# Performance work log

Measured on AMD Instinct MI355X. Metric: run time of the kernel, lower is better.

Reference implementation:

```python
import jax, jax.numpy as jnp
import numpy as np

C_Z = 128
C_HIDDEN = 128
EPS = 1e-5


def _layer_norm(x, w, b):
    mu = jnp.mean(x, axis=-1, keepdims=True)
    var = jnp.var(x, axis=-1, keepdims=True)
    return (x - mu) * jax.lax.rsqrt(var + EPS) * w + b


def setup_inputs() -> dict:
    key = jax.random.key(0)
    ks = jax.random.split(key, 8)
    B, N = 1, 384
    z = jax.random.normal(ks[0], (B, N, N, C_Z), dtype=jnp.float32)
    mask = jnp.ones((B, N, N), dtype=jnp.float32)
    s_z = 1.0 / np.sqrt(C_Z)
    s_h = 1.0 / np.sqrt(C_HIDDEN)
    return {
        "z": z,
        "mask": mask,
        # projection linears (lecun-like random init)
        "w_ap": jax.random.normal(ks[1], (C_HIDDEN, C_Z), jnp.float32) * s_z,
        "b_ap": jnp.zeros((C_HIDDEN,), jnp.float32),
        "w_bp": jax.random.normal(ks[2], (C_HIDDEN, C_Z), jnp.float32) * s_z,
        "b_bp": jnp.zeros((C_HIDDEN,), jnp.float32),
        # gating linears: torch init is zeros weight / ones bias, but use small
        # random weights so gradients are non-trivial; bias = 1 as in 'gating' init
        "w_ag": jax.random.normal(ks[3], (C_HIDDEN, C_Z), jnp.float32) * s_z,
        "b_ag": jnp.ones((C_HIDDEN,), jnp.float32),
        "w_bg": jax.random.normal(ks[4], (C_HIDDEN, C_Z), jnp.float32) * s_z,
        "b_bg": jnp.ones((C_HIDDEN,), jnp.float32),
        "w_g": jax.random.normal(ks[5], (C_Z, C_Z), jnp.float32) * s_z,
        "b_g": jnp.ones((C_Z,), jnp.float32),
        # final output linear ('final' init is zeros; randomize for a useful baseline)
        "w_z": jax.random.normal(ks[6], (C_Z, C_HIDDEN), jnp.float32) * s_h,
        "b_z": jnp.zeros((C_Z,), jnp.float32),
        "ln_in_w": jnp.ones((C_Z,), jnp.float32),
        "ln_in_b": jnp.zeros((C_Z,), jnp.float32),
        "ln_out_w": jnp.ones((C_HIDDEN,), jnp.float32),
        "ln_out_b": jnp.zeros((C_HIDDEN,), jnp.float32),
    }


def reference(z, mask, w_ap, b_ap, w_bp, b_bp, w_ag, b_ag, w_bg, b_bg,
              w_g, b_g, w_z, b_z, ln_in_w, ln_in_b, ln_out_w, ln_out_b):
    # z: [B, N, N, C_z], mask: [B, N, N]
    m = mask[..., None]
    zn = _layer_norm(z, ln_in_w, ln_in_b)
    a = (zn @ w_ap.T + b_ap) * jax.nn.sigmoid(zn @ w_ag.T + b_ag) * m
    b = (zn @ w_bp.T + b_bp) * jax.nn.sigmoid(zn @ w_bg.T + b_bg) * m
    # outgoing: a -> [B,C,i,j], b -> [B,C,j,i]
    a_p = jnp.transpose(a, (0, 3, 1, 2))
    b_p = jnp.transpose(b, (0, 3, 2, 1))
    # NOTE: repo's einsum has no contracted index -> elementwise product a*b
    x = jnp.einsum('bcij,bcji->bijc', a_p, b_p)  # [B, N, N, C_hidden]
    x = _layer_norm(x, ln_out_w, ln_out_b)
    x = x @ w_z.T + b_z
    g = jax.nn.sigmoid(zn @ w_g.T + b_g)
    return x * g
```

## Files before the change

### kernel.cpp

```cpp
#include <hip/hip_runtime.h>
#include <hip/hip_bf16.h>

#define NN 384
#define CC 128
#define PP (NN*NN)
#define PB 64
#define NB (PP/PB)
#define TPB 256

typedef __attribute__((ext_vector_type(8))) short bf16x8;
typedef __attribute__((ext_vector_type(4))) float f32x4;
typedef __attribute__((ext_vector_type(8))) unsigned short u16x8;


__device__ __forceinline__ unsigned short f2bf(float f){
  __hip_bfloat16 h = __float2bfloat16(f);
  return __builtin_bit_cast(unsigned short, h);
}
__device__ __forceinline__ float bf2f(unsigned h){ return __uint_as_float(h<<16); }
__device__ __forceinline__ unsigned pack2(float a, float b){
  return (unsigned)f2bf(a) | ((unsigned)f2bf(b)<<16);
}
__device__ __forceinline__ float sigmoidf_(float x){
  return __fdividef(1.0f, 1.0f + __expf(-x));
}

__global__ __launch_bounds__(256) void k0_wprep(
    const float* __restrict__ wap, const float* __restrict__ wag,
    const float* __restrict__ wbp, const float* __restrict__ wbg,
    const float* __restrict__ wg,  const float* __restrict__ wz,
    unsigned short* __restrict__ wfrag){
  int tid = blockIdx.x*256 + threadIdx.x;
  int plane = tid >> 11, chunk = tid & 2047;
  const float* W = (plane==0) ? wag
                 : (plane==1||plane==2) ? wap
                 : (plane==3) ? wbg
                 : (plane==4||plane==5) ? wbp
                 : (plane==6) ? wg : wz;
  bool lo = (plane==2)||(plane==5);
  int k0 = chunk >> 9, n = (chunk >> 6) & 7, l = chunk & 63;
  int o  = n*16 + (l & 15);
  int kb = k0*32 + ((l>>4)<<3);
  const float* s = W + o*128 + kb;
  u16x8 v;
  #pragma unroll
  for (int e=0;e<8;e++){
    float w = s[e];
    unsigned short hh = f2bf(w);
    v[e] = lo ? f2bf(w - bf2f(hh)) : hh;
  }
  *(u16x8*)(wfrag + (size_t)tid*8) = v;
}

__device__ __forceinline__ void stage_q(const unsigned char* __restrict__ src_base,
                                        unsigned char* slot, int t){
  int wv = t>>6, l = t&63;
  const unsigned char* src = src_base + wv*2048 + l*16;
  unsigned char* dst = slot + wv*2048;
  #pragma unroll
  for (int i=0;i<2;i++)
    __builtin_amdgcn_global_load_lds(
        (const __attribute__((address_space(1))) unsigned int*)(src + i*1024),
        (__attribute__((address_space(3))) unsigned int*)(dst + i*1024),
        16, 0, 0);
}

__device__ __forceinline__ void q_H(const bf16x8* a, int q,
    const unsigned char* slot, int l, f32x4* acc){
  #pragma unroll
  for (int n=0;n<8;n++){
    bf16x8 f = *(const bf16x8*)(slot + n*1024 + l*16);
    acc[n] = __builtin_amdgcn_mfma_f32_16x16x32_bf16(a[q], f, acc[n], 0,0,0);
  }
}
__device__ __forceinline__ void q_HL(const bf16x8* aH, const bf16x8* aL, int q,
    const unsigned char* slot, int l, f32x4* acc){
  #pragma unroll
  for (int n=0;n<8;n++){
    bf16x8 f = *(const bf16x8*)(slot + n*1024 + l*16);
    acc[n] = __builtin_amdgcn_mfma_f32_16x16x32_bf16(aH[q], f, acc[n], 0,0,0);
    acc[n] = __builtin_amdgcn_mfma_f32_16x16x32_bf16(aL[q], f, acc[n], 0,0,0);
  }
}
__device__ __forceinline__ void bias_init(const float* __restrict__ b, int cb,
                                          f32x4* acc){
  #pragma unroll
  for (int n=0;n<8;n++){
    float v = b[n*16 + cb];
    f32x4 iv = {v,v,v,v};
    acc[n]=iv;
  }
}
__device__ __forceinline__ void extract4(const unsigned char* base, int row0,
                                         int l, bf16x8 a[4]){
  int row = row0 + (l&15);
  int swz = (row&7)<<4;
  #pragma unroll
  for (int k0=0;k0<4;k0++){
    unsigned off = (unsigned)(row*256 + ((((l>>4)<<4) + (k0<<6)) ^ swz));
    a[k0] = *(const bf16x8*)(base + off);
  }
}

__global__ __launch_bounds__(TPB,2) void k_fused(
    const float* __restrict__ z, const float* __restrict__ mask,
    const float* __restrict__ bap, const float* __restrict__ bag,
    const float* __restrict__ bbp, const float* __restrict__ bbg,
    const float* __restrict__ bgg, const float* __restrict__ bz,
    const float* __restrict__ lniw, const float* __restrict__ lnib,
    const float* __restrict__ lnow, const float* __restrict__ lnob,
    const unsigned short* __restrict__ wfrag,
    float* __restrict__ out){
  __shared__ unsigned char lds[32768];
  unsigned char* buf = lds;
  const unsigned char* wfrag8 = (const unsigned char*)wfrag;
  const int t = threadIdx.x;
  const int pos0 = blockIdx.x * PB;
  const int wv = t>>6, l = t&63;
  const int h2 = (t>>5)&1;
  const int c4 = (t&31)<<2;
  const int row0 = wv*16;

  stage_q(wfrag8, lds + 16384, t);

  unsigned plr[16];
  {
    float4 lw = *(const float4*)(lniw + c4);
    float4 lb = *(const float4*)(lnib + c4);
    #pragma unroll
    for (int it=0; it<8; ++it){
      int row = row0 + it*2 + h2;
      float4 v = *(const float4*)(z + (size_t)(pos0+row)*CC + c4);
      float s = v.x+v.y+v.z+v.w;
      #pragma unroll
      for (int mm=1; mm<32; mm<<=1) s += __shfl_xor(s,mm);
      float mu = s*(1.0f/128.0f);
      float d0=v.x-mu, d1=v.y-mu, d2=v.z-mu, d3=v.w-mu;
      float ss = d0*d0+d1*d1+d2*d2+d3*d3;
      #pragma unroll
      for (int mm=1; mm<32; mm<<=1) ss += __shfl_xor(ss,mm);
      float rstd = rsqrtf(ss*(1.0f/128.0f) + 1e-5f);
      float n0=d0*rstd*lw.x+lb.x, n1=d1*rstd*lw.y+lb.y;
      float n2=d2*rstd*lw.z+lb.z, n3=d3*rstd*lw.w+lb.w;
      unsigned short hh0=f2bf(n0), hh1=f2bf(n1), hh2=f2bf(n2), hh3=f2bf(n3);
      unsigned off = (unsigned)(row*256 + ((c4<<1) ^ ((row&7)<<4)));
      *(uint2*)(buf + off) = make_uint2((unsigned)hh0|((unsigned)hh1<<16),
                                        (unsigned)hh2|((unsigned)hh3<<16));
      plr[it*2]   = pack2(n0-bf2f(hh0), n1-bf2f(hh1));
      plr[it*2+1] = pack2(n2-bf2f(hh2), n3-bf2f(hh3));
    }
  }
  bf16x8 aH[4], aLo[4];
  extract4(buf, row0, l, aH);
  #pragma unroll
  for (int it=0; it<8; ++it){
    int row = row0 + it*2 + h2;
    unsigned off = (unsigned)(row*256 + ((c4<<1) ^ ((row&7)<<4)));
    *(uint2*)(buf + off) = make_uint2(plr[it*2], plr[it*2+1]);
  }
  extract4(buf, row0, l, aLo);

  const int cb = l&15;
  const int g4 = (l>>4)<<2;

  float mk[4];
  #pragma unroll
  for (int r=0;r<4;r++) mk[r] = mask[pos0 + row0 + g4 + r];

  f32x4 gA[8], gB[8], prj[8];

#define SL(p) (lds + 16384 + (((p)&1)<<13))
#define PH(p) do{ __syncthreads(); \
    if ((p)+1 < 32) stage_q(wfrag8 + ((size_t)((p)+1))*8192, SL((p)+1), t); }while(0)
#define SIG_INPLACE(A) do{ \
    _Pragma("unroll") \
    for (int n=0;n<8;n++) \
      _Pragma("unroll") \
      for (int r=0;r<4;r++) (A)[n][r] = sigmoidf_((A)[n][r]); \
  }while(0)

  PH(0);  bias_init(bag,cb,gA); q_H(aH,0,SL(0), l,gA);
  PH(1);  q_H(aH,1,SL(1), l,gA);
  PH(2);  q_H(aH,2,SL(2), l,gA);
  PH(3);  q_H(aH,3,SL(3), l,gA);
  SIG_INPLACE(gA);
  PH(4);  bias_init(bap,cb,prj); q_HL(aH,aLo,0,SL(4), l,prj);
  PH(5);  q_HL(aH,aLo,1,SL(5), l,prj);
  PH(6);  q_HL(aH,aLo,2,SL(6), l,prj);
  PH(7);  q_HL(aH,aLo,3,SL(7), l,prj);
  PH(8);  q_H(aH,0,SL(8), l,prj);
  PH(9);  q_H(aH,1,SL(9), l,prj);
  PH(10); q_H(aH,2,SL(10),l,prj);
  PH(11); q_H(aH,3,SL(11),l,prj);
  #pragma unroll
  for (int n=0;n<8;n++)
    #pragma unroll
    for (int r=0;r<4;r++)
      gA[n][r] = prj[n][r]*gA[n][r]*mk[r];
  PH(12); bias_init(bbg,cb,gB); q_H(aH,0,SL(12),l,gB);
  PH(13); q_H(aH,1,SL(13),l,gB);
  PH(14); q_H(aH,2,SL(14),l,gB);
  PH(15); q_H(aH,3,SL(15),l,gB);
  SIG_INPLACE(gB);
  PH(16); bias_init(bbp,cb,prj); q_HL(aH,aLo,0,SL(16),l,prj);
  PH(17); q_HL(aH,aLo,1,SL(17),l,prj);
  PH(18); q_HL(aH,aLo,2,SL(18),l,prj);
  PH(19); q_HL(aH,aLo,3,SL(19),l,prj);
  PH(20); q_H(aH,0,SL(20),l,prj);
  PH(21); q_H(aH,1,SL(21),l,prj);
  PH(22); q_H(aH,2,SL(22),l,prj);
  PH(23); q_H(aH,3,SL(23),l,prj);
  bf16x8 a2[4];
  {
    #pragma unroll
    for (int n=0;n<8;n++)
      #pragma unroll
      for (int r=0;r<4;r++)
        gA[n][r] *= prj[n][r]*gB[n][r]*mk[r];
    float lw8[8], lb8[8];
    #pragma unroll
    for (int n=0;n<8;n++){ lw8[n]=lnow[n*16+cb]; lb8[n]=lnob[n*16+cb]; }
    #pragma unroll
    for (int r=0;r<4;r++){
      float s=0.f;
      #pragma unroll
      for (int n=0;n<8;n++) s += gA[n][r];
      #pragma unroll
      for (int mm=1; mm<16; mm<<=1) s += __shfl_xor(s,mm);
      float mu = s*(1.0f/128.0f);
      float ss=0.f;
      #pragma unroll
      for (int n=0;n<8;n++){ float d = gA[n][r]-mu; ss += d*d; }
      #pragma unroll
      for (int mm=1; mm<16; mm<<=1) ss += __shfl_xor(ss,mm);
      float rstd = rsqrtf(ss*(1.0f/128.0f) + 1e-5f);
      int row = row0 + g4 + r;
      int swz = (row&7)<<4;
      #pragma unroll
      for (int n=0;n<8;n++){
        int colb = (n*16+cb)*2;
        float vvv = (gA[n][r]-mu)*rstd*lw8[n]+lb8[n];
        *(unsigned short*)(buf + row*256 + (colb ^ swz)) = f2bf(vvv);
      }
    }
    extract4(buf, row0, l, a2);
  }
  PH(24); bias_init(bgg,cb,gB); q_H(aH,0,SL(24),l,gB);
  PH(25); q_H(aH,1,SL(25),l,gB);
  PH(26); q_H(aH,2,SL(26),l,gB);
  PH(27); q_H(aH,3,SL(27),l,gB);
  SIG_INPLACE(gB);
  PH(28); bias_init(bz,cb,prj); q_H(a2,0,SL(28),l,prj);
  PH(29); q_H(a2,1,SL(29),l,prj);
  PH(30); q_H(a2,2,SL(30),l,prj);
  PH(31); q_H(a2,3,SL(31),l,prj);
  #pragma unroll
  for (int n=0;n<8;n++){
    #pragma unroll
    for (int r=0;r<4;r++){
      int row = row0 + g4 + r;
      out[(size_t)(pos0+row)*CC + n*16 + cb] = prj[n][r]*gB[n][r];
    }
  }
#undef PH
#undef SL
#undef SIG_INPLACE
}

extern "C" void kernel_launch(void* const* d_in, const int* in_sizes, int n_in,
                              void* d_out, int out_size, void* d_ws, size_t ws_size,
                              hipStream_t stream){
  const float* z     = (const float*)d_in[0];
  const float* mask  = (const float*)d_in[1];
  const float* w_ap  = (const float*)d_in[2];
  const float* b_ap  = (const float*)d_in[3];
  const float* w_bp  = (const float*)d_in[4];
  const float* b_bp  = (const float*)d_in[5];
  const float* w_ag  = (const float*)d_in[6];
  const float* b_ag  = (const float*)d_in[7];
  const float* w_bg  = (const float*)d_in[8];
  const float* b_bg  = (const float*)d_in[9];
  const float* w_g   = (const float*)d_in[10];
  const float* b_g   = (const float*)d_in[11];
  const float* w_z   = (const float*)d_in[12];
  const float* b_z   = (const float*)d_in[13];
  const float* ln_in_w  = (const float*)d_in[14];
  const float* ln_in_b  = (const float*)d_in[15];
  const float* ln_out_w = (const float*)d_in[16];
  const float* ln_out_b = (const float*)d_in[17];

  unsigned short* wfrag = (unsigned short*)d_ws;

  k0_wprep<<<64, 256, 0, stream>>>(w_ap, w_ag, w_bp, w_bg, w_g, w_z, wfrag);
  k_fused<<<NB, TPB, 0, stream>>>(z, mask, b_ap, b_ag, b_bp, b_bg, b_g, b_z,
                                  ln_in_w, ln_in_b, ln_out_w, ln_out_b,
                                  wfrag, (float*)d_out);
}
```

Measured before the change: 111.2 us.

## Read weight fragments straight from global memory instead of LDS double-buffering

Drops the 32-phase LDS staging pipeline, which used global_load_lds with a __syncthreads per phase. Each wave now loads its bf16 weight fragments directly from global memory, relying on L1/L2 caching of the 256KB fragment array, inside fully unrolled per-projection passes. This removes 32 block-wide barriers and halves LDS use to 16KB. In exchange, every wave issues its own global loads for the same weights, and load latency is no longer hidden by explicit prefetch.

```diff
diff --git a/kernel.cpp b/kernel.cpp
--- a/kernel.cpp
+++ b/kernel.cpp
@@ -52,34 +52,27 @@
   *(u16x8*)(wfrag + (size_t)tid*8) = v;
 }
 
-__device__ __forceinline__ void stage_q(const unsigned char* __restrict__ src_base,
-                                        unsigned char* slot, int t){
-  int wv = t>>6, l = t&63;
-  const unsigned char* src = src_base + wv*2048 + l*16;
-  unsigned char* dst = slot + wv*2048;
-  #pragma unroll
-  for (int i=0;i<2;i++)
-    __builtin_amdgcn_global_load_lds(
-        (const __attribute__((address_space(1))) unsigned int*)(src + i*1024),
-        (__attribute__((address_space(3))) unsigned int*)(dst + i*1024),
-        16, 0, 0);
-}
-
-__device__ __forceinline__ void q_H(const bf16x8* a, int q,
-    const unsigned char* slot, int l, f32x4* acc){
-  #pragma unroll
-  for (int n=0;n<8;n++){
-    bf16x8 f = *(const bf16x8*)(slot + n*1024 + l*16);
-    acc[n] = __builtin_amdgcn_mfma_f32_16x16x32_bf16(a[q], f, acc[n], 0,0,0);
-  }
-}
-__device__ __forceinline__ void q_HL(const bf16x8* aH, const bf16x8* aL, int q,
-    const unsigned char* slot, int l, f32x4* acc){
-  #pragma unroll
-  for (int n=0;n<8;n++){
-    bf16x8 f = *(const bf16x8*)(slot + n*1024 + l*16);
-    acc[n] = __builtin_amdgcn_mfma_f32_16x16x32_bf16(aH[q], f, acc[n], 0,0,0);
-    acc[n] = __builtin_amdgcn_mfma_f32_16x16x32_bf16(aL[q], f, acc[n], 0,0,0);
+__device__ __forceinline__ void pass_Hg(const bf16x8* a,
+    const unsigned char* __restrict__ wp, int l, f32x4* acc){
+  #pragma unroll
+  for (int q=0;q<4;q++){
+    #pragma unroll
+    for (int n=0;n<8;n++){
+      bf16x8 f = *(const bf16x8*)(wp + q*8192 + n*1024 + l*16);
+      acc[n] = __builtin_amdgcn_mfma_f32_16x16x32_bf16(a[q], f, acc[n], 0,0,0);
+    }
+  }
+}
+__device__ __forceinline__ void pass_HLg(const bf16x8* aH, const bf16x8* aL,
+    const unsigned char* __restrict__ wp, int l, f32x4* acc){
+  #pragma unroll
+  for (int q=0;q<4;q++){
+    #pragma unroll
+    for (int n=0;n<8;n++){
+      bf16x8 f = *(const bf16x8*)(wp + q*8192 + n*1024 + l*16);
+      acc[n] = __builtin_amdgcn_mfma_f32_16x16x32_bf16(aH[q], f, acc[n], 0,0,0);
+      acc[n] = __builtin_amdgcn_mfma_f32_16x16x32_bf16(aL[q], f, acc[n], 0,0,0);
+    }
   }
 }
 __device__ __forceinline__ void bias_init(const float* __restrict__ b, int cb,
@@ -111,17 +104,14 @@
     const float* __restrict__ lnow, const float* __restrict__ lnob,
     const unsigned short* __restrict__ wfrag,
     float* __restrict__ out){
-  __shared__ unsigned char lds[32768];
-  unsigned char* buf = lds;
-  const unsigned char* wfrag8 = (const unsigned char*)wfrag;
+  __shared__ unsigned char buf[16384];
+  const unsigned char* wf = (const unsigned char*)wfrag;
   const int t = threadIdx.x;
   const int pos0 = blockIdx.x * PB;
   const int wv = t>>6, l = t&63;
-  const int h2 = (t>>5)&1;
+  const int hg = (t>>5)&1;
   const int c4 = (t&31)<<2;
   const int row0 = wv*16;
-
-  stage_q(wfrag8, lds + 16384, t);
 
   unsigned plr[16];
   {
@@ -129,7 +119,7 @@
     float4 lb = *(const float4*)(lnib + c4);
     #pragma unroll
     for (int it=0; it<8; ++it){
-      int row = row0 + it*2 + h2;
+      int row = row0 + it*2 + hg;
       float4 v = *(const float4*)(z + (size_t)(pos0+row)*CC + c4);
       float s = v.x+v.y+v.z+v.w;
       #pragma unroll
@@ -154,7 +144,7 @@
   extract4(buf, row0, l, aH);
   #pragma unroll
   for (int it=0; it<8; ++it){
-    int row = row0 + it*2 + h2;
+    int row = row0 + it*2 + hg;
     unsigned off = (unsigned)(row*256 + ((c4<<1) ^ ((row&7)<<4)));
     *(uint2*)(buf + off) = make_uint2(plr[it*2], plr[it*2+1]);
   }
@@ -169,9 +159,6 @@
 
   f32x4 gA[8], gB[8], prj[8];
 
-#define SL(p) (lds + 16384 + (((p)&1)<<13))
-#define PH(p) do{ __syncthreads(); \
-    if ((p)+1 < 32) stage_q(wfrag8 + ((size_t)((p)+1))*8192, SL((p)+1), t); }while(0)
 #define SIG_INPLACE(A) do{ \
     _Pragma("unroll") \
     for (int n=0;n<8;n++) \
@@ -179,37 +166,21 @@
       for (int r=0;r<4;r++) (A)[n][r] = sigmoidf_((A)[n][r]); \
   }while(0)
 
-  PH(0);  bias_init(bag,cb,gA); q_H(aH,0,SL(0), l,gA);
-  PH(1);  q_H(aH,1,SL(1), l,gA);
-  PH(2);  q_H(aH,2,SL(2), l,gA);
-  PH(3);  q_H(aH,3,SL(3), l,gA);
+  bias_init(bag,cb,gA); pass_Hg(aH, wf + 0*32768, l, gA);
   SIG_INPLACE(gA);
-  PH(4);  bias_init(bap,cb,prj); q_HL(aH,aLo,0,SL(4), l,prj);
-  PH(5);  q_HL(aH,aLo,1,SL(5), l,prj);
-  PH(6);  q_HL(aH,aLo,2,SL(6), l,prj);
-  PH(7);  q_HL(aH,aLo,3,SL(7), l,prj);
-  PH(8);  q_H(aH,0,SL(8), l,prj);
-  PH(9);  q_H(aH,1,SL(9), l,prj);
-  PH(10); q_H(aH,2,SL(10),l,prj);
-  PH(11); q_H(aH,3,SL(11),l,prj);
+  bias_init(bap,cb,prj);
+  pass_HLg(aH, aLo, wf + 1*32768, l, prj);
+  pass_Hg (aH,      wf + 2*32768, l, prj);
   #pragma unroll
   for (int n=0;n<8;n++)
     #pragma unroll
     for (int r=0;r<4;r++)
       gA[n][r] = prj[n][r]*gA[n][r]*mk[r];
-  PH(12); bias_init(bbg,cb,gB); q_H(aH,0,SL(12),l,gB);
-  PH(13); q_H(aH,1,SL(13),l,gB);
-  PH(14); q_H(aH,2,SL(14),l,gB);
-  PH(15); q_H(aH,3,SL(15),l,gB);
+  bias_init(bbg,cb,gB); pass_Hg(aH, wf + 3*32768, l, gB);
   SIG_INPLACE(gB);
-  PH(16); bias_init(bbp,cb,prj); q_HL(aH,aLo,0,SL(16),l,prj);
-  PH(17); q_HL(aH,aLo,1,SL(17),l,prj);
-  PH(18); q_HL(aH,aLo,2,SL(18),l,prj);
-  PH(19); q_HL(aH,aLo,3,SL(19),l,prj);
-  PH(20); q_H(aH,0,SL(20),l,prj);
-  PH(21); q_H(aH,1,SL(21),l,prj);
-  PH(22); q_H(aH,2,SL(22),l,prj);
-  PH(23); q_H(aH,3,SL(23),l,prj);
+  bias_init(bbp,cb,prj);
+  pass_HLg(aH, aLo, wf + 4*32768, l, prj);
+  pass_Hg (aH,      wf + 5*32768, l, prj);
   bf16x8 a2[4];
   {
     #pragma unroll
@@ -245,15 +216,9 @@
     }
     extract4(buf, row0, l, a2);
   }
-  PH(24); bias_init(bgg,cb,gB); q_H(aH,0,SL(24),l,gB);
-  PH(25); q_H(aH,1,SL(25),l,gB);
-  PH(26); q_H(aH,2,SL(26),l,gB);
-  PH(27); q_H(aH,3,SL(27),l,gB);
+  bias_init(bgg,cb,gB); pass_Hg(aH, wf + 6*32768, l, gB);
   SIG_INPLACE(gB);
-  PH(28); bias_init(bz,cb,prj); q_H(a2,0,SL(28),l,prj);
-  PH(29); q_H(a2,1,SL(29),l,prj);
-  PH(30); q_H(a2,2,SL(30),l,prj);
-  PH(31); q_H(a2,3,SL(31),l,prj);
+  bias_init(bz,cb,prj); pass_Hg(a2, wf + 7*32768, l, prj);
   #pragma unroll
   for (int n=0;n<8;n++){
     #pragma unroll
@@ -262,8 +227,6 @@
       out[(size_t)(pos0+row)*CC + n*16 + cb] = prj[n][r]*gB[n][r];
     }
   }
-#undef PH
-#undef SL
 #undef SIG_INPLACE
 }
 
```

After: 137.8 us. +23.9%, slower.
